# Optimization experiments

Hardware: AMD Instinct MI355X
Metric: run time of the kernel (lower is better)

Reference implementation:

```python
import jax, jax.numpy as jnp
import numpy as np

N_NODES = 100000
N_EDGES = 1600000
N_FEAT = 16
HEADS = 4


def _feast_conv(x, src, dst, U, c, W, b):
    """FeaStConv: q = softmax_h(u^T(x_j - x_i) + c); out_i = mean_j sum_h q_h * (W_h x_j) + b."""
    n = x.shape[0]
    e = src.shape[0]
    xj = x[src]                                   # [E, Fin] gather
    q = jax.nn.softmax(jnp.matmul(xj - x[dst], U) + c, axis=-1)   # [E, H]
    xs = jnp.matmul(xj, W).reshape(e, HEADS, -1)  # [E, H, Fout]
    msg = jnp.einsum('eh,eho->eo', q, xs)         # [E, Fout]
    deg = jax.ops.segment_sum(jnp.ones((e,), x.dtype), dst, num_segments=n)
    agg = jax.ops.segment_sum(msg, dst, num_segments=n)
    return agg / jnp.maximum(deg, 1.0)[:, None] + b


def setup_inputs() -> dict:
    key = jax.random.key(0)
    ks = jax.random.split(key, 32)
    s = 0.1
    d = {
        'x': jax.random.normal(ks[0], (N_NODES, N_FEAT), jnp.float32),
        'edge_index': jax.random.randint(ks[1], (2, N_EDGES), 0, N_NODES, jnp.int32),
        # conv1: 16 -> 16
        'U1': jax.random.normal(ks[2], (N_FEAT, HEADS), jnp.float32) * s,
        'c1': jnp.zeros((HEADS,), jnp.float32),
        'W1': jax.random.normal(ks[3], (N_FEAT, HEADS * 16), jnp.float32) * s,
        'b1': jnp.zeros((16,), jnp.float32),
        # conv2: 16 -> 32
        'U2': jax.random.normal(ks[4], (16, HEADS), jnp.float32) * s,
        'c2': jnp.zeros((HEADS,), jnp.float32),
        'W2': jax.random.normal(ks[5], (16, HEADS * 32), jnp.float32) * s,
        'b2': jnp.zeros((32,), jnp.float32),
        # conv3: 32 -> 64
        'U3': jax.random.normal(ks[6], (32, HEADS), jnp.float32) * s,
        'c3': jnp.zeros((HEADS,), jnp.float32),
        'W3': jax.random.normal(ks[7], (32, HEADS * 64), jnp.float32) * s,
        'b3': jnp.zeros((64,), jnp.float32),
        # linear tail 64->32->16->8->4->1
        'lw1': jax.random.normal(ks[8], (64, 32), jnp.float32) * s,
        'lb1': jnp.zeros((32,), jnp.float32),
        'lw2': jax.random.normal(ks[9], (32, 16), jnp.float32) * s,
        'lb2': jnp.zeros((16,), jnp.float32),
        'lw3': jax.random.normal(ks[10], (16, 8), jnp.float32) * s,
        'lb3': jnp.zeros((8,), jnp.float32),
        'lw4': jax.random.normal(ks[11], (8, 4), jnp.float32) * s,
        'lb4': jnp.zeros((4,), jnp.float32),
        'lw5': jax.random.normal(ks[12], (4, 1), jnp.float32) * s,
        'lb5': jnp.zeros((1,), jnp.float32),
    }
    return d


def reference(x, edge_index, U1, c1, W1, b1, U2, c2, W2, b2, U3, c3, W3, b3,
              lw1, lb1, lw2, lb2, lw3, lb3, lw4, lb4, lw5, lb5):
    src, dst = edge_index[0], edge_index[1]
    h = jax.nn.relu(_feast_conv(x, src, dst, U1, c1, W1, b1))
    h = jax.nn.relu(_feast_conv(h, src, dst, U2, c2, W2, b2))
    h = jax.nn.relu(_feast_conv(h, src, dst, U3, c3, W3, b3))
    # dropout disabled (inference / drop_bool=False): Linear+ReLU tail
    h = jax.nn.relu(jnp.matmul(h, lw1) + lb1)
    h = jax.nn.relu(jnp.matmul(h, lw2) + lb2)
    h = jax.nn.relu(jnp.matmul(h, lw3) + lb3)
    h = jax.nn.relu(jnp.matmul(h, lw4) + lb4)
    return jax.nn.sigmoid(jnp.matmul(h, lw5) + lb5)   # [N, 1]
```

## Files before the change

### kernel.cpp

```cpp
#include <hip/hip_runtime.h>
#include <math.h>

#define N_NODES 100000
#define N_EDGES 1600000
#define HEADS 4
#define NBKT ((N_NODES + 255) / 256)
#define CHUNK_E 4096
#define NCHUNK ((N_EDGES + CHUNK_E - 1) / CHUNK_E)


__global__ void zero_int_kernel(int* __restrict__ ptr, int n) {
    int i = blockIdx.x * blockDim.x + threadIdx.x;
    if (i < n) ptr[i] = 0;
}

__global__ __launch_bounds__(256) void bhist_kernel(const int* __restrict__ dst,
                                                    int* __restrict__ bucket_cnt) {
    __shared__ int h[NBKT];
    for (int i = threadIdx.x; i < NBKT; i += 256) h[i] = 0;
    __syncthreads();
    int base = blockIdx.x * CHUNK_E;
    #pragma unroll
    for (int j = 0; j < CHUNK_E / 256; j++) {
        int e = base + j * 256 + threadIdx.x;
        if (e < N_EDGES) atomicAdd(&h[dst[e] >> 8], 1);
    }
    __syncthreads();
    for (int i = threadIdx.x; i < NBKT; i += 256)
        if (h[i]) atomicAdd(&bucket_cnt[i], h[i]);
}

__global__ __launch_bounds__(512) void bscan_kernel(const int* __restrict__ bucket_cnt,
                                                    int* __restrict__ bucket_base,
                                                    int* __restrict__ bucket_cursor) {
    __shared__ int tmp[512];
    int i = threadIdx.x;
    int v = (i < NBKT) ? bucket_cnt[i] : 0;
    tmp[i] = v;
    __syncthreads();
    for (int off = 1; off < 512; off <<= 1) {
        int t = (i >= off) ? tmp[i - off] : 0;
        __syncthreads();
        tmp[i] += t;
        __syncthreads();
    }
    int excl = tmp[i] - v;
    if (i < NBKT) { bucket_base[i] = excl; bucket_cursor[i] = excl; }
    if (i == NBKT) bucket_base[NBKT] = N_EDGES;
}

__global__ __launch_bounds__(256) void partition_kernel(const int* __restrict__ src,
                                                        const int* __restrict__ dst,
                                                        int* __restrict__ bucket_cursor,
                                                        int* __restrict__ csr_tmp) {
    constexpr int EPT = CHUNK_E / 256;
    __shared__ int h[NBKT];
    __shared__ int gbase[NBKT];
    __shared__ int rcnt[NBKT];
    for (int i = threadIdx.x; i < NBKT; i += 256) { h[i] = 0; rcnt[i] = 0; }
    __syncthreads();
    int base = blockIdx.x * CHUNK_E;
    int d[EPT], s[EPT];
    #pragma unroll
    for (int j = 0; j < EPT; j++) {
        int e = base + j * 256 + threadIdx.x;
        d[j] = (e < N_EDGES) ? dst[e] : -1;
        s[j] = (e < N_EDGES) ? src[e] : 0;
        if (d[j] >= 0) atomicAdd(&h[d[j] >> 8], 1);
    }
    __syncthreads();
    for (int i = threadIdx.x; i < NBKT; i += 256)
        if (h[i]) gbase[i] = atomicAdd(&bucket_cursor[i], h[i]);
    __syncthreads();
    #pragma unroll
    for (int j = 0; j < EPT; j++) {
        if (d[j] >= 0) {
            int b = d[j] >> 8;
            int r = atomicAdd(&rcnt[b], 1);
            csr_tmp[gbase[b] + r] = ((d[j] & 255) << 20) | s[j];
        }
    }
}

__global__ __launch_bounds__(256) void bucket_build_kernel(const int* __restrict__ bucket_base,
                                                           const int* __restrict__ csr_tmp,
                                                           int* __restrict__ rowptr,
                                                           int* __restrict__ csr_src) {
    __shared__ int cnt[256];
    __shared__ int tscan[256];
    __shared__ int exc[256];
    __shared__ int stage[8192];
    int b = blockIdx.x;
    int rbeg = bucket_base[b], rend = bucket_base[b + 1];
    int sz = rend - rbeg;
    int tid = threadIdx.x;

    cnt[tid] = 0;
    __syncthreads();
    for (int k = rbeg + tid; k < rend; k += 256) atomicAdd(&cnt[csr_tmp[k] >> 20], 1);
    __syncthreads();
    int v = cnt[tid];
    tscan[tid] = v;
    __syncthreads();
    for (int off = 1; off < 256; off <<= 1) {
        int t = (tid >= off) ? tscan[tid - off] : 0;
        __syncthreads();
        tscan[tid] += t;
        __syncthreads();
    }
    int ex = tscan[tid] - v;
    int node = b * 256 + tid;
    if (node < N_NODES) rowptr[node] = rbeg + ex;
    if (b == 0 && tid == 0) rowptr[N_NODES] = N_EDGES;
    exc[tid] = ex;
    cnt[tid] = 0;
    __syncthreads();

    if (sz <= 8192) {
        for (int k = rbeg + tid; k < rend; k += 256) {
            int pk = csr_tmp[k];
            int dl = pk >> 20;
            int r  = atomicAdd(&cnt[dl], 1);
            stage[exc[dl] + r] = pk & ((1 << 20) - 1);
        }
        __syncthreads();
        for (int i = tid; i < sz; i += 256) csr_src[rbeg + i] = stage[i];
    } else {
        for (int k = rbeg + tid; k < rend; k += 256) {
            int pk = csr_tmp[k];
            int dl = pk >> 20;
            int r  = atomicAdd(&cnt[dl], 1);
            csr_src[rbeg + exc[dl] + r] = pk & ((1 << 20) - 1);
        }
    }
}


template<int FIN>
__global__ __launch_bounds__(256) void p_kernel(
        const float* __restrict__ h, const float* __restrict__ U,
        float* __restrict__ p)
{
    int n = blockIdx.x * blockDim.x + threadIdx.x;
    if (n >= N_NODES) return;
    float a0 = 0, a1 = 0, a2 = 0, a3 = 0;
    const float* hr = h + (size_t)n * FIN;
    #pragma unroll
    for (int f = 0; f < FIN; f++) {
        float xv = hr[f];
        a0 += xv * U[f * 4 + 0];
        a1 += xv * U[f * 4 + 1];
        a2 += xv * U[f * 4 + 2];
        a3 += xv * U[f * 4 + 3];
    }
    *(float4*)(p + (size_t)n * 4) = make_float4(a0, a1, a2, a3);
}


template<int FIN>
__global__ __launch_bounds__(256) void zgather_kernel(
        const int* __restrict__ rowptr, const int* __restrict__ csr_src,
        const float* __restrict__ p,
        const float* __restrict__ cvec,
        const float* __restrict__ hprev,
        float* __restrict__ z)
{
    constexpr int NPB   = 256 / FIN;
    constexpr int CHUNK = 512;
    __shared__ int    sbeg[NPB + 1];
    __shared__ float4 qs[CHUNK];
    __shared__ int    ssrc[CHUNK];

    int tid  = threadIdx.x;
    int nloc = tid / FIN;
    int f    = tid - nloc * FIN;
    int n0   = blockIdx.x * NPB;
    int n    = n0 + nloc;

    if (tid <= NPB) {
        int idx = n0 + tid;
        sbeg[tid] = rowptr[idx > N_NODES ? N_NODES : idx];
    }
    float c0 = cvec[0], c1 = cvec[1], c2 = cvec[2], c3 = cvec[3];
    __syncthreads();

    int BB = sbeg[0], BE = sbeg[NPB];
    int beg = sbeg[nloc], end = sbeg[nloc + 1];

    float a0 = 0, a1 = 0, a2 = 0, a3 = 0;

    for (int cbase = BB; cbase < BE; cbase += CHUNK) {
        int cend = min(cbase + CHUNK, BE);
        __syncthreads();
        for (int k = cbase + tid; k < cend; k += 256) {
            int s = csr_src[k];
            int lo = 0, hi = NPB;
            while (hi - lo > 1) { int mid = (lo + hi) >> 1; if (k < sbeg[mid]) hi = mid; else lo = mid; }
            float4 ps = *(const float4*)(p + (size_t)s * 4);
            float4 pd = *(const float4*)(p + (size_t)(n0 + lo) * 4);
            float l0 = ps.x - pd.x + c0;
            float l1 = ps.y - pd.y + c1;
            float l2 = ps.z - pd.z + c2;
            float l3 = ps.w - pd.w + c3;
            float m  = fmaxf(fmaxf(l0, l1), fmaxf(l2, l3));
            float e0 = __expf(l0 - m), e1 = __expf(l1 - m);
            float e2 = __expf(l2 - m), e3 = __expf(l3 - m);
            float deg = (float)(sbeg[lo + 1] - sbeg[lo]);
            float inv = 1.0f / (fmaxf(deg, 1.0f) * (e0 + e1 + e2 + e3));
            qs[k - cbase]   = make_float4(e0 * inv, e1 * inv, e2 * inv, e3 * inv);
            ssrc[k - cbase] = s;
        }
        __syncthreads();
        int kb = (beg > cbase ? beg : cbase) - cbase;
        int ke = (end < cend ? end : cend) - cbase;
        int k = kb;
        for (; k + 4 <= ke; k += 4) {
            int s0 = ssrc[k], s1 = ssrc[k + 1], s2 = ssrc[k + 2], s3 = ssrc[k + 3];
            float x0 = hprev[(size_t)s0 * FIN + f];
            float x1 = hprev[(size_t)s1 * FIN + f];
            float x2 = hprev[(size_t)s2 * FIN + f];
            float x3 = hprev[(size_t)s3 * FIN + f];
            float4 q0 = qs[k], q1 = qs[k + 1], q2 = qs[k + 2], q3 = qs[k + 3];
            a0 += q0.x * x0; a1 += q0.y * x0; a2 += q0.z * x0; a3 += q0.w * x0;
            a0 += q1.x * x1; a1 += q1.y * x1; a2 += q1.z * x1; a3 += q1.w * x1;
            a0 += q2.x * x2; a1 += q2.y * x2; a2 += q2.z * x2; a3 += q2.w * x2;
            a0 += q3.x * x3; a1 += q3.y * x3; a2 += q3.z * x3; a3 += q3.w * x3;
        }
        for (; k < ke; k++) {
            int s    = ssrc[k];
            float4 q = qs[k];
            float xv = hprev[(size_t)s * FIN + f];
            a0 += q.x * xv; a1 += q.y * xv; a2 += q.z * xv; a3 += q.w * xv;
        }
    }

    if (n < N_NODES) {
        size_t base = (size_t)n * (4 * FIN) + f;
        z[base]           = a0;
        z[base + FIN]     = a1;
        z[base + 2 * FIN] = a2;
        z[base + 3 * FIN] = a3;
    }
}


template<int FIN, int FOUT>
__global__ __launch_bounds__(256, 4) void post_kernel(
        const float* __restrict__ z,
        const float* __restrict__ W,
        const float* __restrict__ b,
        float* __restrict__ out)
{
    constexpr int K   = 4 * FIN;
    constexpr int OL  = FOUT / 4;
    constexpr int NPB = 4 * (256 / OL);
    constexpr int WSZ = FIN * 4 * FOUT;
    __shared__ float Wp[WSZ];
    for (int i = threadIdx.x; i < WSZ; i += 256) {
        int f = i / (4 * FOUT);
        int r = i - f * (4 * FOUT);
        int h = r / FOUT;
        int o = r - h * FOUT;
        Wp[(h * FIN + f) * FOUT + o] = W[i];
    }
    __syncthreads();

    int ol = threadIdx.x % OL;
    int g  = threadIdx.x / OL;
    int n0 = blockIdx.x * NPB + g * 4;

    float4 bv = *(const float4*)(b + 4 * ol);
    float4 acc[4];
    const float* zr[4];
    #pragma unroll
    for (int j = 0; j < 4; j++) {
        acc[j] = make_float4(0.f, 0.f, 0.f, 0.f);
        int nn = n0 + j; if (nn > N_NODES - 1) nn = N_NODES - 1;
        zr[j] = z + (size_t)nn * K;
    }

    #pragma unroll 2
    for (int kq = 0; kq < K / 4; kq++) {
        float4 zv[4];
        #pragma unroll
        for (int j = 0; j < 4; j++)
            zv[j] = *(const float4*)(zr[j] + 4 * kq);
        #pragma unroll
        for (int jj = 0; jj < 4; jj++) {
            float4 wv = *(const float4*)(Wp + (4 * kq + jj) * FOUT + 4 * ol);
            #pragma unroll
            for (int j = 0; j < 4; j++) {
                float s = (&zv[j].x)[jj];
                acc[j].x += s * wv.x;
                acc[j].y += s * wv.y;
                acc[j].z += s * wv.z;
                acc[j].w += s * wv.w;
            }
        }
    }

    #pragma unroll
    for (int j = 0; j < 4; j++) {
        int nn = n0 + j;
        if (nn < N_NODES) {
            float4 r;
            r.x = fmaxf(acc[j].x + bv.x, 0.0f);
            r.y = fmaxf(acc[j].y + bv.y, 0.0f);
            r.z = fmaxf(acc[j].z + bv.z, 0.0f);
            r.w = fmaxf(acc[j].w + bv.w, 0.0f);
            *(float4*)(out + (size_t)nn * FOUT + 4 * ol) = r;
        }
    }
}


__global__ __launch_bounds__(256) void tail_kernel(
        const float* __restrict__ h,
        const float* __restrict__ lw1, const float* __restrict__ lb1,
        const float* __restrict__ lw2, const float* __restrict__ lb2,
        const float* __restrict__ lw3, const float* __restrict__ lb3,
        const float* __restrict__ lw4, const float* __restrict__ lb4,
        const float* __restrict__ lw5, const float* __restrict__ lb5,
        float* __restrict__ out)
{
    __shared__ float w1[64 * 32], w2[32 * 16], w3[16 * 8], w4[8 * 4], w5[4];
    __shared__ float B1[32], B2[16], B3[8], B4[4], B5[1];
    for (int i = threadIdx.x; i < 64 * 32; i += blockDim.x) w1[i] = lw1[i];
    for (int i = threadIdx.x; i < 32 * 16; i += blockDim.x) w2[i] = lw2[i];
    for (int i = threadIdx.x; i < 16 * 8;  i += blockDim.x) w3[i] = lw3[i];
    for (int i = threadIdx.x; i < 8 * 4;   i += blockDim.x) w4[i] = lw4[i];
    for (int i = threadIdx.x; i < 4;       i += blockDim.x) w5[i] = lw5[i];
    for (int i = threadIdx.x; i < 32; i += blockDim.x) B1[i] = lb1[i];
    for (int i = threadIdx.x; i < 16; i += blockDim.x) B2[i] = lb2[i];
    for (int i = threadIdx.x; i < 8;  i += blockDim.x) B3[i] = lb3[i];
    for (int i = threadIdx.x; i < 4;  i += blockDim.x) B4[i] = lb4[i];
    if (threadIdx.x == 0) B5[0] = lb5[0];
    __syncthreads();

    int n = blockIdx.x * blockDim.x + threadIdx.x;
    if (n >= N_NODES) return;

    float a[64];
    #pragma unroll
    for (int i = 0; i < 64; i++) a[i] = h[(size_t)n * 64 + i];

    float t1[32];
    for (int o = 0; o < 32; o++) {
        float acc = B1[o];
        #pragma unroll
        for (int i = 0; i < 64; i++) acc += a[i] * w1[i * 32 + o];
        t1[o] = fmaxf(acc, 0.0f);
    }
    float t2[16];
    for (int o = 0; o < 16; o++) {
        float acc = B2[o];
        #pragma unroll
        for (int i = 0; i < 32; i++) acc += t1[i] * w2[i * 16 + o];
        t2[o] = fmaxf(acc, 0.0f);
    }
    float t3[8];
    for (int o = 0; o < 8; o++) {
        float acc = B3[o];
        #pragma unroll
        for (int i = 0; i < 16; i++) acc += t2[i] * w3[i * 8 + o];
        t3[o] = fmaxf(acc, 0.0f);
    }
    float t4[4];
    for (int o = 0; o < 4; o++) {
        float acc = B4[o];
        #pragma unroll
        for (int i = 0; i < 8; i++) acc += t3[i] * w4[i * 4 + o];
        t4[o] = fmaxf(acc, 0.0f);
    }
    float zf = B5[0];
    #pragma unroll
    for (int i = 0; i < 4; i++) zf += t4[i] * w5[i];
    out[n] = 1.0f / (1.0f + expf(-zf));
}


extern "C" void kernel_launch(void* const* d_in, const int* in_sizes, int n_in,
                              void* d_out, int out_size, void* d_ws, size_t ws_size,
                              hipStream_t stream) {
    const float* x   = (const float*)d_in[0];
    const int*   ei  = (const int*)d_in[1];
    const int*   src = ei;
    const int*   dst = ei + N_EDGES;
    const float* U1 = (const float*)d_in[2];  const float* c1 = (const float*)d_in[3];
    const float* W1 = (const float*)d_in[4];  const float* b1 = (const float*)d_in[5];
    const float* U2 = (const float*)d_in[6];  const float* c2 = (const float*)d_in[7];
    const float* W2 = (const float*)d_in[8];  const float* b2 = (const float*)d_in[9];
    const float* U3 = (const float*)d_in[10]; const float* c3 = (const float*)d_in[11];
    const float* W3 = (const float*)d_in[12]; const float* b3 = (const float*)d_in[13];
    const float* lw1 = (const float*)d_in[14]; const float* lb1 = (const float*)d_in[15];
    const float* lw2 = (const float*)d_in[16]; const float* lb2 = (const float*)d_in[17];
    const float* lw3 = (const float*)d_in[18]; const float* lb3 = (const float*)d_in[19];
    const float* lw4 = (const float*)d_in[20]; const float* lb4 = (const float*)d_in[21];
    const float* lw5 = (const float*)d_in[22]; const float* lb5 = (const float*)d_in[23];

    char* ws = (char*)d_ws;
    size_t off = 0;
    auto alloc = [&](size_t bytes) -> void* {
        void* ptr = (void*)(ws + off);
        off += (bytes + 255) & ~(size_t)255;
        return ptr;
    };
    int*    bucket_cnt    = (int*)alloc((size_t)(NBKT + 1) * 4);
    int*    bucket_base   = (int*)alloc((size_t)(NBKT + 1) * 4);
    int*    bucket_cursor = (int*)alloc((size_t)NBKT * 4);
    int*    csr_tmp       = (int*)alloc((size_t)N_EDGES * 4);
    int*    rowptr        = (int*)alloc(((size_t)N_NODES + 1) * 4);
    int*    csr_src       = (int*)alloc((size_t)N_EDGES * 4);
    float*  p             = (float*)alloc((size_t)N_NODES * 4 * 4);
    float*  z             = (float*)alloc((size_t)N_NODES * 128 * 4);
    float*  h1            = (float*)alloc((size_t)N_NODES * 16 * 4);
    float*  h2            = (float*)alloc((size_t)N_NODES * 32 * 4);
    float*  h3            = (float*)alloc((size_t)N_NODES * 64 * 4);
    (void)ws_size;

    const int B = 256;
    int gN = (N_NODES + B - 1) / B;

    zero_int_kernel<<<(NBKT + 255) / 256, B, 0, stream>>>(bucket_cnt, NBKT);
    bhist_kernel<<<NCHUNK, B, 0, stream>>>(dst, bucket_cnt);
    bscan_kernel<<<1, 512, 0, stream>>>(bucket_cnt, bucket_base, bucket_cursor);
    partition_kernel<<<NCHUNK, B, 0, stream>>>(src, dst, bucket_cursor, csr_tmp);
    bucket_build_kernel<<<NBKT, B, 0, stream>>>(bucket_base, csr_tmp, rowptr, csr_src);

    const int ZG16 = (N_NODES + (256 / 16) - 1) / (256 / 16);
    const int ZG32 = (N_NODES + (256 / 32) - 1) / (256 / 32);
    const int NPB1 = 4 * (256 / (16 / 4));
    const int NPB2 = 4 * (256 / (32 / 4));
    const int NPB3 = 4 * (256 / (64 / 4));

    p_kernel<16><<<gN, B, 0, stream>>>(x, U1, p);
    zgather_kernel<16><<<ZG16, B, 0, stream>>>(rowptr, csr_src, p, c1, x, z);
    post_kernel<16, 16><<<(N_NODES + NPB1 - 1) / NPB1, B, 0, stream>>>(z, W1, b1, h1);

    p_kernel<16><<<gN, B, 0, stream>>>(h1, U2, p);
    zgather_kernel<16><<<ZG16, B, 0, stream>>>(rowptr, csr_src, p, c2, h1, z);
    post_kernel<16, 32><<<(N_NODES + NPB2 - 1) / NPB2, B, 0, stream>>>(z, W2, b2, h2);

    p_kernel<32><<<gN, B, 0, stream>>>(h2, U3, p);
    zgather_kernel<32><<<ZG32, B, 0, stream>>>(rowptr, csr_src, p, c3, h2, z);
    post_kernel<32, 64><<<(N_NODES + NPB3 - 1) / NPB3, B, 0, stream>>>(z, W3, b3, h3);

    tail_kernel<<<gN, B, 0, stream>>>(h3, lw1, lb1, lw2, lb2, lw3, lb3,
                                      lw4, lb4, lw5, lb5, (float*)d_out);
}
```

Baseline: 364.6 us.

## Fuse next-layer attention projection into post kernel and store layer-2 features as bf16

The post kernel now also computes the next layer's per-node attention projection (h·U) from a shared-memory tile, which removes two separate p_kernel launches and their re-read of the hidden features. Layer-2 output is written as bf16, and a new gather kernel reads bf16 source features with 4-way unrolled accumulation, halving the bytes of the irregular neighbor gather for layer 3. In exchange, layer-3 inputs lose precision, and the post kernel uses extra shared memory and an added sync.

```diff
diff --git a/kernel.cpp b/kernel.cpp
--- a/kernel.cpp
+++ b/kernel.cpp
@@ -7,6 +7,17 @@
 #define NBKT ((N_NODES + 255) / 256)
 #define CHUNK_E 4096
 #define NCHUNK ((N_EDGES + CHUNK_E - 1) / CHUNK_E)
+
+typedef unsigned short ushort_t;
+
+__device__ __forceinline__ ushort_t f2bf(float x) {
+    unsigned u = __float_as_uint(x);
+    u += 0x7FFF + ((u >> 16) & 1);
+    return (ushort_t)(u >> 16);
+}
+__device__ __forceinline__ float bf2f(ushort_t v) {
+    return __uint_as_float(((unsigned)v) << 16);
+}
 
 
 __global__ void zero_int_kernel(int* __restrict__ ptr, int n) {
@@ -160,8 +171,7 @@
 template<int FIN>
 __global__ __launch_bounds__(256) void zgather_kernel(
         const int* __restrict__ rowptr, const int* __restrict__ csr_src,
-        const float* __restrict__ p,
-        const float* __restrict__ cvec,
+        const float* __restrict__ p, const float* __restrict__ cvec,
         const float* __restrict__ hprev,
         float* __restrict__ z)
 {
@@ -186,7 +196,6 @@
 
     int BB = sbeg[0], BE = sbeg[NPB];
     int beg = sbeg[nloc], end = sbeg[nloc + 1];
-
     float a0 = 0, a1 = 0, a2 = 0, a3 = 0;
 
     for (int cbase = BB; cbase < BE; cbase += CHUNK) {
@@ -244,24 +253,118 @@
 }
 
 
-template<int FIN, int FOUT>
+template<int FIN>
+__global__ __launch_bounds__(256) void zgather_bf16_kernel(
+        const int* __restrict__ rowptr, const int* __restrict__ csr_src,
+        const float* __restrict__ p, const float* __restrict__ cvec,
+        const ushort_t* __restrict__ hprev,
+        float* __restrict__ z)
+{
+    constexpr int NPB   = 256 / FIN;
+    constexpr int CHUNK = 512;
+    __shared__ int    sbeg[NPB + 1];
+    __shared__ float4 qs[CHUNK];
+    __shared__ int    ssrc[CHUNK];
+
+    int tid  = threadIdx.x;
+    int nloc = tid / FIN;
+    int f    = tid - nloc * FIN;
+    int n0   = blockIdx.x * NPB;
+    int n    = n0 + nloc;
+
+    if (tid <= NPB) {
+        int idx = n0 + tid;
+        sbeg[tid] = rowptr[idx > N_NODES ? N_NODES : idx];
+    }
+    float c0 = cvec[0], c1 = cvec[1], c2 = cvec[2], c3 = cvec[3];
+    __syncthreads();
+
+    int BB = sbeg[0], BE = sbeg[NPB];
+    int beg = sbeg[nloc], end = sbeg[nloc + 1];
+    float a0 = 0, a1 = 0, a2 = 0, a3 = 0;
+
+    for (int cbase = BB; cbase < BE; cbase += CHUNK) {
+        int cend = min(cbase + CHUNK, BE);
+        __syncthreads();
+        for (int k = cbase + tid; k < cend; k += 256) {
+            int s = csr_src[k];
+            int lo = 0, hi = NPB;
+            while (hi - lo > 1) { int mid = (lo + hi) >> 1; if (k < sbeg[mid]) hi = mid; else lo = mid; }
+            float4 ps = *(const float4*)(p + (size_t)s * 4);
+            float4 pd = *(const float4*)(p + (size_t)(n0 + lo) * 4);
+            float l0 = ps.x - pd.x + c0;
+            float l1 = ps.y - pd.y + c1;
+            float l2 = ps.z - pd.z + c2;
+            float l3 = ps.w - pd.w + c3;
+            float m  = fmaxf(fmaxf(l0, l1), fmaxf(l2, l3));
+            float e0 = __expf(l0 - m), e1 = __expf(l1 - m);
+            float e2 = __expf(l2 - m), e3 = __expf(l3 - m);
+            float deg = (float)(sbeg[lo + 1] - sbeg[lo]);
+            float inv = 1.0f / (fmaxf(deg, 1.0f) * (e0 + e1 + e2 + e3));
+            qs[k - cbase]   = make_float4(e0 * inv, e1 * inv, e2 * inv, e3 * inv);
+            ssrc[k - cbase] = s;
+        }
+        __syncthreads();
+        int kb = (beg > cbase ? beg : cbase) - cbase;
+        int ke = (end < cend ? end : cend) - cbase;
+        int k = kb;
+        for (; k + 4 <= ke; k += 4) {
+            int s0 = ssrc[k], s1 = ssrc[k + 1], s2 = ssrc[k + 2], s3 = ssrc[k + 3];
+            ushort_t u0 = hprev[(size_t)s0 * FIN + f];
+            ushort_t u1 = hprev[(size_t)s1 * FIN + f];
+            ushort_t u2 = hprev[(size_t)s2 * FIN + f];
+            ushort_t u3 = hprev[(size_t)s3 * FIN + f];
+            float x0 = bf2f(u0), x1 = bf2f(u1), x2 = bf2f(u2), x3 = bf2f(u3);
+            float4 q0 = qs[k], q1 = qs[k + 1], q2 = qs[k + 2], q3 = qs[k + 3];
+            a0 += q0.x * x0; a1 += q0.y * x0; a2 += q0.z * x0; a3 += q0.w * x0;
+            a0 += q1.x * x1; a1 += q1.y * x1; a2 += q1.z * x1; a3 += q1.w * x1;
+            a0 += q2.x * x2; a1 += q2.y * x2; a2 += q2.z * x2; a3 += q2.w * x2;
+            a0 += q3.x * x3; a1 += q3.y * x3; a2 += q3.z * x3; a3 += q3.w * x3;
+        }
+        for (; k < ke; k++) {
+            int s    = ssrc[k];
+            float4 q = qs[k];
+            float xv = bf2f(hprev[(size_t)s * FIN + f]);
+            a0 += q.x * xv; a1 += q.y * xv; a2 += q.z * xv; a3 += q.w * xv;
+        }
+    }
+
+    if (n < N_NODES) {
+        size_t base = (size_t)n * (4 * FIN) + f;
+        z[base]           = a0;
+        z[base + FIN]     = a1;
+        z[base + 2 * FIN] = a2;
+        z[base + 3 * FIN] = a3;
+    }
+}
+
+
+template<int FIN, int FOUT, int MODE>
 __global__ __launch_bounds__(256, 4) void post_kernel(
         const float* __restrict__ z,
         const float* __restrict__ W,
         const float* __restrict__ b,
-        float* __restrict__ out)
+        float* __restrict__ out,
+        ushort_t* __restrict__ out_bf,
+        const float* __restrict__ Unext,
+        float* __restrict__ pnext)
 {
     constexpr int K   = 4 * FIN;
     constexpr int OL  = FOUT / 4;
     constexpr int NPB = 4 * (256 / OL);
     constexpr int WSZ = FIN * 4 * FOUT;
     __shared__ float Wp[WSZ];
+    __shared__ float htile[MODE ? NPB * FOUT : 1];
+    __shared__ float Uloc[MODE ? FOUT * 4 : 1];
     for (int i = threadIdx.x; i < WSZ; i += 256) {
         int f = i / (4 * FOUT);
         int r = i - f * (4 * FOUT);
         int h = r / FOUT;
         int o = r - h * FOUT;
         Wp[(h * FIN + f) * FOUT + o] = W[i];
+    }
+    if (MODE) {
+        for (int i = threadIdx.x; i < FOUT * 4; i += 256) Uloc[i] = Unext[i];
     }
     __syncthreads();
 
@@ -302,13 +405,42 @@
     #pragma unroll
     for (int j = 0; j < 4; j++) {
         int nn = n0 + j;
+        float4 r;
+        r.x = fmaxf(acc[j].x + bv.x, 0.0f);
+        r.y = fmaxf(acc[j].y + bv.y, 0.0f);
+        r.z = fmaxf(acc[j].z + bv.z, 0.0f);
+        r.w = fmaxf(acc[j].w + bv.w, 0.0f);
+        if (MODE)
+            *(float4*)(htile + (g * 4 + j) * FOUT + 4 * ol) = r;
         if (nn < N_NODES) {
-            float4 r;
-            r.x = fmaxf(acc[j].x + bv.x, 0.0f);
-            r.y = fmaxf(acc[j].y + bv.y, 0.0f);
-            r.z = fmaxf(acc[j].z + bv.z, 0.0f);
-            r.w = fmaxf(acc[j].w + bv.w, 0.0f);
-            *(float4*)(out + (size_t)nn * FOUT + 4 * ol) = r;
+            if (MODE == 2) {
+                ushort4 u;
+                u.x = f2bf(r.x); u.y = f2bf(r.y); u.z = f2bf(r.z); u.w = f2bf(r.w);
+                *(ushort4*)(out_bf + (size_t)nn * FOUT + 4 * ol) = u;
+            } else {
+                *(float4*)(out + (size_t)nn * FOUT + 4 * ol) = r;
+            }
+        }
+    }
+
+    if (MODE) {
+        __syncthreads();
+        int tid = threadIdx.x;
+        if (tid < NPB) {
+            int nn = blockIdx.x * NPB + tid;
+            if (nn < N_NODES) {
+                float a0 = 0, a1 = 0, a2 = 0, a3 = 0;
+                const float* hr = htile + tid * FOUT;
+                #pragma unroll
+                for (int f = 0; f < FOUT; f++) {
+                    float xv = hr[f];
+                    a0 += xv * Uloc[f * 4 + 0];
+                    a1 += xv * Uloc[f * 4 + 1];
+                    a2 += xv * Uloc[f * 4 + 2];
+                    a3 += xv * Uloc[f * 4 + 3];
+                }
+                *(float4*)(pnext + (size_t)nn * 4) = make_float4(a0, a1, a2, a3);
+            }
         }
     }
 }
@@ -405,17 +537,17 @@
         off += (bytes + 255) & ~(size_t)255;
         return ptr;
     };
-    int*    bucket_cnt    = (int*)alloc((size_t)(NBKT + 1) * 4);
-    int*    bucket_base   = (int*)alloc((size_t)(NBKT + 1) * 4);
-    int*    bucket_cursor = (int*)alloc((size_t)NBKT * 4);
-    int*    csr_tmp       = (int*)alloc((size_t)N_EDGES * 4);
-    int*    rowptr        = (int*)alloc(((size_t)N_NODES + 1) * 4);
-    int*    csr_src       = (int*)alloc((size_t)N_EDGES * 4);
-    float*  p             = (float*)alloc((size_t)N_NODES * 4 * 4);
-    float*  z             = (float*)alloc((size_t)N_NODES * 128 * 4);
-    float*  h1            = (float*)alloc((size_t)N_NODES * 16 * 4);
-    float*  h2            = (float*)alloc((size_t)N_NODES * 32 * 4);
-    float*  h3            = (float*)alloc((size_t)N_NODES * 64 * 4);
+    int*      bucket_cnt    = (int*)alloc((size_t)(NBKT + 1) * 4);
+    int*      bucket_base   = (int*)alloc((size_t)(NBKT + 1) * 4);
+    int*      bucket_cursor = (int*)alloc((size_t)NBKT * 4);
+    int*      csr_tmp       = (int*)alloc((size_t)N_EDGES * 4);
+    int*      rowptr        = (int*)alloc(((size_t)N_NODES + 1) * 4);
+    int*      csr_src       = (int*)alloc((size_t)N_EDGES * 4);
+    float*    p             = (float*)alloc((size_t)N_NODES * 4 * 4);
+    float*    z             = (float*)alloc((size_t)N_NODES * 128 * 4);
+    float*    h1            = (float*)alloc((size_t)N_NODES * 16 * 4);
+    ushort_t* h2bf          = (ushort_t*)alloc((size_t)N_NODES * 32 * 2);
+    float*    h3            = (float*)alloc((size_t)N_NODES * 64 * 4);
     (void)ws_size;
 
     const int B = 256;
@@ -435,15 +567,16 @@
 
     p_kernel<16><<<gN, B, 0, stream>>>(x, U1, p);
     zgather_kernel<16><<<ZG16, B, 0, stream>>>(rowptr, csr_src, p, c1, x, z);
-    post_kernel<16, 16><<<(N_NODES + NPB1 - 1) / NPB1, B, 0, stream>>>(z, W1, b1, h1);
-
-    p_kernel<16><<<gN, B, 0, stream>>>(h1, U2, p);
+    post_kernel<16, 16, 1><<<(N_NODES + NPB1 - 1) / NPB1, B, 0, stream>>>(
+        z, W1, b1, h1, nullptr, U2, p);
+
     zgather_kernel<16><<<ZG16, B, 0, stream>>>(rowptr, csr_src, p, c2, h1, z);
-    post_kernel<16, 32><<<(N_NODES + NPB2 - 1) / NPB2, B, 0, stream>>>(z, W2, b2, h2);
-
-    p_kernel<32><<<gN, B, 0, stream>>>(h2, U3, p);
-    zgather_kernel<32><<<ZG32, B, 0, stream>>>(rowptr, csr_src, p, c3, h2, z);
-    post_kernel<32, 64><<<(N_NODES + NPB3 - 1) / NPB3, B, 0, stream>>>(z, W3, b3, h3);
+    post_kernel<16, 32, 2><<<(N_NODES + NPB2 - 1) / NPB2, B, 0, stream>>>(
+        z, W2, b2, nullptr, h2bf, U3, p);
+
+    zgather_bf16_kernel<32><<<ZG32, B, 0, stream>>>(rowptr, csr_src, p, c3, h2bf, z);
+    post_kernel<32, 64, 0><<<(N_NODES + NPB3 - 1) / NPB3, B, 0, stream>>>(
+        z, W3, b3, h3, nullptr, nullptr, nullptr);
 
     tail_kernel<<<gN, B, 0, stream>>>(h3, lw1, lb1, lw2, lb2, lw3, lb3,
                                       lw4, lb4, lw5, lb5, (float*)d_out);
```

Measured after the change: 355.2 us. 2.6% less time.

## Store node features in bf16 and fuse next-layer attention projection into post kernel

Applied to the files above, without the earlier changes.

Node features (input x and each layer's output) are now stored as bf16. This halves the bytes moved by the random per-edge gathers in zgather and by the tail kernel's reads, while accumulation stays in fp32. The post kernel also computes the next layer's attention projection p = h·U from an fp32 tile in shared memory, which removes the separate p_kernel launches and their re-read of h. The cost is reduced precision of the gathered features, which adds rounding error relative to the fp32 reference.

```diff
diff --git a/kernel.cpp b/kernel.cpp
--- a/kernel.cpp
+++ b/kernel.cpp
@@ -7,6 +7,21 @@
 #define NBKT ((N_NODES + 255) / 256)
 #define CHUNK_E 4096
 #define NCHUNK ((N_EDGES + CHUNK_E - 1) / CHUNK_E)
+
+typedef unsigned short ushort_t;
+
+__device__ __forceinline__ ushort_t f2bf(float x) {
+    unsigned u = __float_as_uint(x);
+    u += 0x7FFF + ((u >> 16) & 1);
+    return (ushort_t)(u >> 16);
+}
+__device__ __forceinline__ float bf2f(ushort_t v) {
+    return __uint_as_float(((unsigned)v) << 16);
+}
+__device__ __forceinline__ void unpack2(unsigned u, float& lo, float& hi) {
+    lo = __uint_as_float(u << 16);
+    hi = __uint_as_float(u & 0xffff0000u);
+}
 
 
 __global__ void zero_int_kernel(int* __restrict__ ptr, int n) {
@@ -136,33 +151,40 @@
 }
 
 
-template<int FIN>
-__global__ __launch_bounds__(256) void p_kernel(
-        const float* __restrict__ h, const float* __restrict__ U,
-        float* __restrict__ p)
+__global__ __launch_bounds__(256) void p_cast_kernel(
+        const float* __restrict__ x, const float* __restrict__ U,
+        float* __restrict__ p,
+        ushort_t* __restrict__ xbf)
 {
     int n = blockIdx.x * blockDim.x + threadIdx.x;
     if (n >= N_NODES) return;
     float a0 = 0, a1 = 0, a2 = 0, a3 = 0;
-    const float* hr = h + (size_t)n * FIN;
-    #pragma unroll
-    for (int f = 0; f < FIN; f++) {
-        float xv = hr[f];
-        a0 += xv * U[f * 4 + 0];
-        a1 += xv * U[f * 4 + 1];
-        a2 += xv * U[f * 4 + 2];
-        a3 += xv * U[f * 4 + 3];
+    const float* hr = x + (size_t)n * 16;
+    float xv[16];
+    #pragma unroll
+    for (int f = 0; f < 16; f++) {
+        xv[f] = hr[f];
+        a0 += xv[f] * U[f * 4 + 0];
+        a1 += xv[f] * U[f * 4 + 1];
+        a2 += xv[f] * U[f * 4 + 2];
+        a3 += xv[f] * U[f * 4 + 3];
     }
     *(float4*)(p + (size_t)n * 4) = make_float4(a0, a1, a2, a3);
+    #pragma unroll
+    for (int j = 0; j < 4; j++) {
+        ushort4 u;
+        u.x = f2bf(xv[4 * j + 0]); u.y = f2bf(xv[4 * j + 1]);
+        u.z = f2bf(xv[4 * j + 2]); u.w = f2bf(xv[4 * j + 3]);
+        *(ushort4*)(xbf + (size_t)n * 16 + 4 * j) = u;
+    }
 }
 
 
 template<int FIN>
-__global__ __launch_bounds__(256) void zgather_kernel(
+__global__ __launch_bounds__(256) void zgather_bf16_kernel(
         const int* __restrict__ rowptr, const int* __restrict__ csr_src,
-        const float* __restrict__ p,
-        const float* __restrict__ cvec,
-        const float* __restrict__ hprev,
+        const float* __restrict__ p, const float* __restrict__ cvec,
+        const ushort_t* __restrict__ hprev,
         float* __restrict__ z)
 {
     constexpr int NPB   = 256 / FIN;
@@ -186,7 +208,6 @@
 
     int BB = sbeg[0], BE = sbeg[NPB];
     int beg = sbeg[nloc], end = sbeg[nloc + 1];
-
     float a0 = 0, a1 = 0, a2 = 0, a3 = 0;
 
     for (int cbase = BB; cbase < BE; cbase += CHUNK) {
@@ -214,22 +235,33 @@
         int kb = (beg > cbase ? beg : cbase) - cbase;
         int ke = (end < cend ? end : cend) - cbase;
         int k = kb;
+        for (; k + 8 <= ke; k += 8) {
+            ushort_t u[8];
+            #pragma unroll
+            for (int j = 0; j < 8; j++)
+                u[j] = hprev[(size_t)ssrc[k + j] * FIN + f];
+            #pragma unroll
+            for (int j = 0; j < 8; j++) {
+                float xv = bf2f(u[j]);
+                float4 q = qs[k + j];
+                a0 += q.x * xv; a1 += q.y * xv; a2 += q.z * xv; a3 += q.w * xv;
+            }
+        }
         for (; k + 4 <= ke; k += 4) {
-            int s0 = ssrc[k], s1 = ssrc[k + 1], s2 = ssrc[k + 2], s3 = ssrc[k + 3];
-            float x0 = hprev[(size_t)s0 * FIN + f];
-            float x1 = hprev[(size_t)s1 * FIN + f];
-            float x2 = hprev[(size_t)s2 * FIN + f];
-            float x3 = hprev[(size_t)s3 * FIN + f];
-            float4 q0 = qs[k], q1 = qs[k + 1], q2 = qs[k + 2], q3 = qs[k + 3];
-            a0 += q0.x * x0; a1 += q0.y * x0; a2 += q0.z * x0; a3 += q0.w * x0;
-            a0 += q1.x * x1; a1 += q1.y * x1; a2 += q1.z * x1; a3 += q1.w * x1;
-            a0 += q2.x * x2; a1 += q2.y * x2; a2 += q2.z * x2; a3 += q2.w * x2;
-            a0 += q3.x * x3; a1 += q3.y * x3; a2 += q3.z * x3; a3 += q3.w * x3;
+            ushort_t u[4];
+            #pragma unroll
+            for (int j = 0; j < 4; j++)
+                u[j] = hprev[(size_t)ssrc[k + j] * FIN + f];
+            #pragma unroll
+            for (int j = 0; j < 4; j++) {
+                float xv = bf2f(u[j]);
+                float4 q = qs[k + j];
+                a0 += q.x * xv; a1 += q.y * xv; a2 += q.z * xv; a3 += q.w * xv;
+            }
         }
         for (; k < ke; k++) {
-            int s    = ssrc[k];
+            float xv = bf2f(hprev[(size_t)ssrc[k] * FIN + f]);
             float4 q = qs[k];
-            float xv = hprev[(size_t)s * FIN + f];
             a0 += q.x * xv; a1 += q.y * xv; a2 += q.z * xv; a3 += q.w * xv;
         }
     }
@@ -244,24 +276,32 @@
 }
 
 
-template<int FIN, int FOUT>
+template<int FIN, int FOUT, int MODE>
 __global__ __launch_bounds__(256, 4) void post_kernel(
         const float* __restrict__ z,
         const float* __restrict__ W,
         const float* __restrict__ b,
-        float* __restrict__ out)
+        ushort_t* __restrict__ out_bf,
+        const float* __restrict__ Unext,
+        float* __restrict__ pnext)
 {
     constexpr int K   = 4 * FIN;
     constexpr int OL  = FOUT / 4;
     constexpr int NPB = 4 * (256 / OL);
     constexpr int WSZ = FIN * 4 * FOUT;
+    constexpr bool PNEXT = (MODE == 2);
     __shared__ float Wp[WSZ];
+    __shared__ float htile[PNEXT ? NPB * FOUT : 1];
+    __shared__ float Uloc[PNEXT ? FOUT * 4 : 1];
     for (int i = threadIdx.x; i < WSZ; i += 256) {
         int f = i / (4 * FOUT);
         int r = i - f * (4 * FOUT);
         int h = r / FOUT;
         int o = r - h * FOUT;
         Wp[(h * FIN + f) * FOUT + o] = W[i];
+    }
+    if (PNEXT) {
+        for (int i = threadIdx.x; i < FOUT * 4; i += 256) Uloc[i] = Unext[i];
     }
     __syncthreads();
 
@@ -302,20 +342,45 @@
     #pragma unroll
     for (int j = 0; j < 4; j++) {
         int nn = n0 + j;
+        float4 r;
+        r.x = fmaxf(acc[j].x + bv.x, 0.0f);
+        r.y = fmaxf(acc[j].y + bv.y, 0.0f);
+        r.z = fmaxf(acc[j].z + bv.z, 0.0f);
+        r.w = fmaxf(acc[j].w + bv.w, 0.0f);
+        if (PNEXT)
+            *(float4*)(htile + (g * 4 + j) * FOUT + 4 * ol) = r;
         if (nn < N_NODES) {
-            float4 r;
-            r.x = fmaxf(acc[j].x + bv.x, 0.0f);
-            r.y = fmaxf(acc[j].y + bv.y, 0.0f);
-            r.z = fmaxf(acc[j].z + bv.z, 0.0f);
-            r.w = fmaxf(acc[j].w + bv.w, 0.0f);
-            *(float4*)(out + (size_t)nn * FOUT + 4 * ol) = r;
+            ushort4 u;
+            u.x = f2bf(r.x); u.y = f2bf(r.y); u.z = f2bf(r.z); u.w = f2bf(r.w);
+            *(ushort4*)(out_bf + (size_t)nn * FOUT + 4 * ol) = u;
+        }
+    }
+
+    if (PNEXT) {
+        __syncthreads();
+        int tid = threadIdx.x;
+        if (tid < NPB) {
+            int nn = blockIdx.x * NPB + tid;
+            if (nn < N_NODES) {
+                float a0 = 0, a1 = 0, a2 = 0, a3 = 0;
+                const float* hr = htile + tid * FOUT;
+                #pragma unroll
+                for (int f = 0; f < FOUT; f++) {
+                    float xv = hr[f];
+                    a0 += xv * Uloc[f * 4 + 0];
+                    a1 += xv * Uloc[f * 4 + 1];
+                    a2 += xv * Uloc[f * 4 + 2];
+                    a3 += xv * Uloc[f * 4 + 3];
+                }
+                *(float4*)(pnext + (size_t)nn * 4) = make_float4(a0, a1, a2, a3);
+            }
         }
     }
 }
 
 
 __global__ __launch_bounds__(256) void tail_kernel(
-        const float* __restrict__ h,
+        const ushort_t* __restrict__ h,
         const float* __restrict__ lw1, const float* __restrict__ lb1,
         const float* __restrict__ lw2, const float* __restrict__ lb2,
         const float* __restrict__ lw3, const float* __restrict__ lb3,
@@ -341,8 +406,15 @@
     if (n >= N_NODES) return;
 
     float a[64];
-    #pragma unroll
-    for (int i = 0; i < 64; i++) a[i] = h[(size_t)n * 64 + i];
+    const uint4* hrow = (const uint4*)(h + (size_t)n * 64);
+    #pragma unroll
+    for (int j = 0; j < 8; j++) {
+        uint4 v = hrow[j];
+        unpack2(v.x, a[8 * j + 0], a[8 * j + 1]);
+        unpack2(v.y, a[8 * j + 2], a[8 * j + 3]);
+        unpack2(v.z, a[8 * j + 4], a[8 * j + 5]);
+        unpack2(v.w, a[8 * j + 6], a[8 * j + 7]);
+    }
 
     float t1[32];
     for (int o = 0; o < 32; o++) {
@@ -405,17 +477,18 @@
         off += (bytes + 255) & ~(size_t)255;
         return ptr;
     };
-    int*    bucket_cnt    = (int*)alloc((size_t)(NBKT + 1) * 4);
-    int*    bucket_base   = (int*)alloc((size_t)(NBKT + 1) * 4);
-    int*    bucket_cursor = (int*)alloc((size_t)NBKT * 4);
-    int*    csr_tmp       = (int*)alloc((size_t)N_EDGES * 4);
-    int*    rowptr        = (int*)alloc(((size_t)N_NODES + 1) * 4);
-    int*    csr_src       = (int*)alloc((size_t)N_EDGES * 4);
-    float*  p             = (float*)alloc((size_t)N_NODES * 4 * 4);
-    float*  z             = (float*)alloc((size_t)N_NODES * 128 * 4);
-    float*  h1            = (float*)alloc((size_t)N_NODES * 16 * 4);
-    float*  h2            = (float*)alloc((size_t)N_NODES * 32 * 4);
-    float*  h3            = (float*)alloc((size_t)N_NODES * 64 * 4);
+    int*      bucket_cnt    = (int*)alloc((size_t)(NBKT + 1) * 4);
+    int*      bucket_base   = (int*)alloc((size_t)(NBKT + 1) * 4);
+    int*      bucket_cursor = (int*)alloc((size_t)NBKT * 4);
+    int*      csr_tmp       = (int*)alloc((size_t)N_EDGES * 4);
+    int*      rowptr        = (int*)alloc(((size_t)N_NODES + 1) * 4);
+    int*      csr_src       = (int*)alloc((size_t)N_EDGES * 4);
+    float*    p             = (float*)alloc((size_t)N_NODES * 4 * 4);
+    float*    z             = (float*)alloc((size_t)N_NODES * 128 * 4);
+    ushort_t* xbf           = (ushort_t*)alloc((size_t)N_NODES * 16 * 2);
+    ushort_t* h1bf          = (ushort_t*)alloc((size_t)N_NODES * 16 * 2);
+    ushort_t* h2bf          = (ushort_t*)alloc((size_t)N_NODES * 32 * 2);
+    ushort_t* h3bf          = (ushort_t*)alloc((size_t)N_NODES * 64 * 2);
     (void)ws_size;
 
     const int B = 256;
@@ -433,18 +506,19 @@
     const int NPB2 = 4 * (256 / (32 / 4));
     const int NPB3 = 4 * (256 / (64 / 4));
 
-    p_kernel<16><<<gN, B, 0, stream>>>(x, U1, p);
-    zgather_kernel<16><<<ZG16, B, 0, stream>>>(rowptr, csr_src, p, c1, x, z);
-    post_kernel<16, 16><<<(N_NODES + NPB1 - 1) / NPB1, B, 0, stream>>>(z, W1, b1, h1);
-
-    p_kernel<16><<<gN, B, 0, stream>>>(h1, U2, p);
-    zgather_kernel<16><<<ZG16, B, 0, stream>>>(rowptr, csr_src, p, c2, h1, z);
-    post_kernel<16, 32><<<(N_NODES + NPB2 - 1) / NPB2, B, 0, stream>>>(z, W2, b2, h2);
-
-    p_kernel<32><<<gN, B, 0, stream>>>(h2, U3, p);
-    zgather_kernel<32><<<ZG32, B, 0, stream>>>(rowptr, csr_src, p, c3, h2, z);
-    post_kernel<32, 64><<<(N_NODES + NPB3 - 1) / NPB3, B, 0, stream>>>(z, W3, b3, h3);
-
-    tail_kernel<<<gN, B, 0, stream>>>(h3, lw1, lb1, lw2, lb2, lw3, lb3,
+    p_cast_kernel<<<gN, B, 0, stream>>>(x, U1, p, xbf);
+    zgather_bf16_kernel<16><<<ZG16, B, 0, stream>>>(rowptr, csr_src, p, c1, xbf, z);
+    post_kernel<16, 16, 2><<<(N_NODES + NPB1 - 1) / NPB1, B, 0, stream>>>(
+        z, W1, b1, h1bf, U2, p);
+
+    zgather_bf16_kernel<16><<<ZG16, B, 0, stream>>>(rowptr, csr_src, p, c2, h1bf, z);
+    post_kernel<16, 32, 2><<<(N_NODES + NPB2 - 1) / NPB2, B, 0, stream>>>(
+        z, W2, b2, h2bf, U3, p);
+
+    zgather_bf16_kernel<32><<<ZG32, B, 0, stream>>>(rowptr, csr_src, p, c3, h2bf, z);
+    post_kernel<32, 64, 3><<<(N_NODES + NPB3 - 1) / NPB3, B, 0, stream>>>(
+        z, W3, b3, h3bf, nullptr, nullptr);
+
+    tail_kernel<<<gN, B, 0, stream>>>(h3bf, lw1, lb1, lw2, lb2, lw3, lb3,
                                       lw4, lb4, lw5, lb5, (float*)d_out);
 }
```

New measurement: 346.3 us. 5.0% less time.
